# Kernel tuning notes

Hardware: AMD Instinct MI355X
Metric: run time of the kernel (lower is better)

The kernel has to match this reference:

```python
import jax, jax.numpy as jnp
import numpy as np

PZ = 16          # partition_size
SMOOTH = 1e-8


def setup_inputs() -> dict:
    key = jax.random.key(0)
    k1, k2, k3, k4 = jax.random.split(key, 4)
    shape = (4, 2, 160, 160, 160)  # [N, C, Z, X, Y]
    pred = jax.random.uniform(k1, shape, dtype=jnp.float32)
    groundtruth = jax.random.uniform(k2, shape, dtype=jnp.float32)
    a = jax.random.uniform(k3, (1,), dtype=jnp.float32)
    b = jax.random.uniform(k4, (1,), dtype=jnp.float32)
    return {"pred": pred, "groundtruth": groundtruth, "a": a, "b": b}


def _blocks(t):
    # [N,C,Z,X,Y] -> rows of per-(block, channel) voxels [N*nz*nx*ny*C, PZ^3]
    # matches the torch loops: blocks ordered (N, zz, xx, yy) with channel dim
    # of each block concatenated along dim 0 before flattening dims 1..-1.
    N, C, Z, X, Y = t.shape
    nz, nx, ny = Z // PZ, X // PZ, Y // PZ
    t = t.reshape(N, C, nz, PZ, nx, PZ, ny, PZ)
    t = t.transpose(0, 2, 4, 6, 1, 3, 5, 7)  # [N,nz,nx,ny,C,pz,pz,pz]
    return t.reshape(N * nz * nx * ny * C, PZ * PZ * PZ)


def reference(pred, groundtruth, a, b):
    p = _blocks(pred)
    g = _blocks(groundtruth)
    tp = jnp.sum(g * p, axis=1)
    fn = jnp.sum(g * (1.0 - p), axis=1)
    fp = jnp.sum((1.0 - g) * p, axis=1)
    denom = fp + fn + SMOOTH
    alpha = a + b * ((fp + SMOOTH) / denom)
    beta = a + b * ((fn + SMOOTH) / denom)
    loss = jnp.sum(1.0 - (tp + SMOOTH) / (tp + alpha * fp + beta * fn + SMOOTH))
    return loss
```

## Files before the change

kernel.cpp:

```cpp
#include <hip/hip_runtime.h>

#define SMOOTH 1e-8f

constexpr int NROWS = 8000;
constexpr int WG1   = 3200;

__global__ __launch_bounds__(256, 8)
void partial_kernel(const float* __restrict__ pred,
                    const float* __restrict__ gt,
                    float* __restrict__ wsq)
{
    int wg = blockIdx.x;
    const int q4 = wg & 3;  wg >>= 2;
    const int c  = wg & 1;  wg >>= 1;
    const int xx = wg % 10; wg /= 10;
    const int zz = wg % 10;
    const int n  = wg / 10;

    const int t  = threadIdx.x;
    const int s  = t & 15;
    const int xl = t >> 4;
    const long base0 =
        ((long)((n * 2 + c) * 160 + zz * 16 + q4 * 4) * 160 + xx * 16) * 40L;

    const float4* p4 = reinterpret_cast<const float4*>(pred);
    const float4* g4 = reinterpret_cast<const float4*>(gt);

    float S0 = 0, G0 = 0, P0 = 0;
    float S1 = 0, G1 = 0, P1 = 0;
    float S2 = 0, G2 = 0, P2 = 0;
    const bool j2 = (s < 8);

    #pragma unroll
    for (int plane = 0; plane < 4; ++plane) {
        const long lb = base0 + (long)plane * 6400 + xl * 40 + s;
        const float4 pa = p4[lb];      const float4 ga = g4[lb];
        const float4 pb = p4[lb + 16]; const float4 gb = g4[lb + 16];
        float4 pc, gc;
        if (j2) { pc = p4[lb + 32]; gc = g4[lb + 32]; }

        S0 += (pa.x + pa.y) + (pa.z + pa.w);
        G0 += (ga.x + ga.y) + (ga.z + ga.w);
        P0 += pa.x * ga.x + pa.y * ga.y + pa.z * ga.z + pa.w * ga.w;

        S1 += (pb.x + pb.y) + (pb.z + pb.w);
        G1 += (gb.x + gb.y) + (gb.z + gb.w);
        P1 += pb.x * gb.x + pb.y * gb.y + pb.z * gb.z + pb.w * gb.w;

        if (j2) {
            S2 += (pc.x + pc.y) + (pc.z + pc.w);
            G2 += (gc.x + gc.y) + (gc.z + gc.w);
            P2 += pc.x * gc.x + pc.y * gc.y + pc.z * gc.z + pc.w * gc.w;
        }
    }

#define RED4(x) x += __shfl_xor(x, 1, 64); x += __shfl_xor(x, 2, 64); \
                x += __shfl_xor(x, 16, 64); x += __shfl_xor(x, 32, 64);
    RED4(S0) RED4(G0) RED4(P0)
    RED4(S1) RED4(G1) RED4(P1)
    RED4(S2) RED4(G2) RED4(P2)
#undef RED4

    __shared__ float red[4][4][9];
    const int lane = t & 63, wave = t >> 6;
    if ((lane & 51) == 0) {
        const int q = lane >> 2;
        float* dst = red[wave][q];
        dst[0] = S0; dst[1] = G0; dst[2] = P0;
        dst[3] = S1; dst[4] = G1; dst[5] = P1;
        dst[6] = S2; dst[7] = G2; dst[8] = P2;
    }
    __syncthreads();

    if (t < 30) {
        const int yy   = t / 3;
        const int comp = t - yy * 3;
        const int q = yy & 3, j = yy >> 2;
        const float val = red[0][q][j * 3 + comp] + red[1][q][j * 3 + comp] +
                          red[2][q][j * 3 + comp] + red[3][q][j * 3 + comp];
        const int row = (((n * 10 + zz) * 10 + xx) * 10 + yy) * 2 + c;
        wsq[(row * 4 + q4) * 3 + comp] = val;
    }
}

__global__ __launch_bounds__(1024)
void finalize_kernel(const float* __restrict__ wsq,
                     const float* __restrict__ a_p,
                     const float* __restrict__ b_p,
                     float* __restrict__ out)
{
    const int t = threadIdx.x;
    const float a = a_p[0], b = b_p[0];
    float sum = 0.f;

    for (int r = t; r < NROWS; r += 1024) {
        const float4 w0 = *reinterpret_cast<const float4*>(wsq + r * 12);
        const float4 w1 = *reinterpret_cast<const float4*>(wsq + r * 12 + 4);
        const float4 w2 = *reinterpret_cast<const float4*>(wsq + r * 12 + 8);
        const float SP  = w0.x + w0.w + w1.z + w2.y;
        const float SG  = w0.y + w1.x + w1.w + w2.z;
        const float SGP = w0.z + w1.y + w2.x + w2.w;

        const float tp = SGP;
        const float fn = SG - SGP;
        const float fp = SP - SGP;
        const float denom = fp + fn + SMOOTH;
        const float alpha = a + b * ((fp + SMOOTH) / denom);
        const float beta  = a + b * ((fn + SMOOTH) / denom);
        sum += 1.f - (tp + SMOOTH) / (tp + alpha * fp + beta * fn + SMOOTH);
    }

    #pragma unroll
    for (int d = 32; d > 0; d >>= 1) sum += __shfl_down(sum, d, 64);

    __shared__ float wsum[16];
    if ((t & 63) == 0) wsum[t >> 6] = sum;
    __syncthreads();
    if (t == 0) {
        float tot = 0.f;
        #pragma unroll
        for (int i = 0; i < 16; ++i) tot += wsum[i];
        out[0] = tot;
    }
}

extern "C" void kernel_launch(void* const* d_in, const int* in_sizes, int n_in,
                              void* d_out, int out_size, void* d_ws, size_t ws_size,
                              hipStream_t stream)
{
    const float* pred = (const float*)d_in[0];
    const float* gt   = (const float*)d_in[1];
    const float* a_p  = (const float*)d_in[2];
    const float* b_p  = (const float*)d_in[3];
    float* out = (float*)d_out;
    float* wsq = (float*)d_ws;

    partial_kernel<<<WG1, 256, 0, stream>>>(pred, gt, wsq);
    finalize_kernel<<<1, 1024, 0, stream>>>(wsq, a_p, b_p, out);
}
```

Baseline: 302.6 us.

## Remap partial reduction so each wave streams one z-plane with nontemporal loads

Each wave now reads one contiguous z-plane slab (16 x-rows of 40 float4s) as 10 fully coalesced 64-lane float4 loads of pred and gt, all issued up front with nontemporal hints. Previously lanes were split by x-row and y-segment, with a predicated third load. The y-block assignment of each lane rotates across the 10 loads, so per-lane partials are regrouped into 5 y-block bins with selects before a cross-lane shuffle reduction and a smaller shared-memory combine. Occupancy hint drops to 4 waves-per-SIMD to allow the 80 live load registers, which trades latency hiding across waves for more memory-level parallelism per wave.

Result: faster. 252.8 us (-16.5%).

```diff
diff --git a/kernel.cpp b/kernel.cpp
--- a/kernel.cpp
+++ b/kernel.cpp
@@ -2,10 +2,12 @@
 
 #define SMOOTH 1e-8f
 
+typedef float f32x4 __attribute__((ext_vector_type(4)));
+
 constexpr int NROWS = 8000;
 constexpr int WG1   = 3200;
 
-__global__ __launch_bounds__(256, 8)
+__global__ __launch_bounds__(256, 4)
 void partial_kernel(const float* __restrict__ pred,
                     const float* __restrict__ gt,
                     float* __restrict__ wsq)
@@ -17,67 +19,83 @@
     const int zz = wg % 10;
     const int n  = wg / 10;
 
-    const int t  = threadIdx.x;
-    const int s  = t & 15;
-    const int xl = t >> 4;
-    const long base0 =
-        ((long)((n * 2 + c) * 160 + zz * 16 + q4 * 4) * 160 + xx * 16) * 40L;
+    const int t    = threadIdx.x;
+    const int lane = t & 63;
+    const int wave = t >> 6;
+    const int z    = zz * 16 + q4 * 4 + wave;
 
-    const float4* p4 = reinterpret_cast<const float4*>(pred);
-    const float4* g4 = reinterpret_cast<const float4*>(gt);
+    const long pb = ((long)((n * 2 + c) * 160 + z) * 160 + xx * 16) * 40L;
 
-    float S0 = 0, G0 = 0, P0 = 0;
-    float S1 = 0, G1 = 0, P1 = 0;
-    float S2 = 0, G2 = 0, P2 = 0;
-    const bool j2 = (s < 8);
+    const f32x4* p4 = reinterpret_cast<const f32x4*>(pred) + pb + lane;
+    const f32x4* g4 = reinterpret_cast<const f32x4*>(gt)  + pb + lane;
+
+    f32x4 P[10], G[10];
+    #pragma unroll
+    for (int k = 0; k < 10; ++k) {
+        P[k] = __builtin_nontemporal_load(p4 + k * 64);
+        G[k] = __builtin_nontemporal_load(g4 + k * 64);
+    }
+
+    float aS[5] = {0, 0, 0, 0, 0};
+    float aG[5] = {0, 0, 0, 0, 0};
+    float aP[5] = {0, 0, 0, 0, 0};
+    #pragma unroll
+    for (int k = 0; k < 10; ++k) {
+        const int m = k % 5;
+        const f32x4 p = P[k], g = G[k];
+        aS[m] += (p.x + p.y) + (p.z + p.w);
+        aG[m] += (g.x + g.y) + (g.z + g.w);
+        aP[m] += p.x * g.x + p.y * g.y + p.z * g.z + p.w * g.w;
+    }
+
+    int rr[5];
+    #pragma unroll
+    for (int m = 0; m < 5; ++m)
+        rr[m] = ((lane + 24 * m) % 40) >> 3;
+
+    float bS[5], bG[5], bP[5];
+    #pragma unroll
+    for (int r = 0; r < 5; ++r) {
+        float s = 0.f, g = 0.f, p = 0.f;
+        #pragma unroll
+        for (int m = 0; m < 5; ++m) {
+            const bool hit = (rr[m] == r);
+            s += hit ? aS[m] : 0.f;
+            g += hit ? aG[m] : 0.f;
+            p += hit ? aP[m] : 0.f;
+        }
+        bS[r] = s; bG[r] = g; bP[r] = p;
+    }
 
     #pragma unroll
-    for (int plane = 0; plane < 4; ++plane) {
-        const long lb = base0 + (long)plane * 6400 + xl * 40 + s;
-        const float4 pa = p4[lb];      const float4 ga = g4[lb];
-        const float4 pb = p4[lb + 16]; const float4 gb = g4[lb + 16];
-        float4 pc, gc;
-        if (j2) { pc = p4[lb + 32]; gc = g4[lb + 32]; }
-
-        S0 += (pa.x + pa.y) + (pa.z + pa.w);
-        G0 += (ga.x + ga.y) + (ga.z + ga.w);
-        P0 += pa.x * ga.x + pa.y * ga.y + pa.z * ga.z + pa.w * ga.w;
-
-        S1 += (pb.x + pb.y) + (pb.z + pb.w);
-        G1 += (gb.x + gb.y) + (gb.z + gb.w);
-        P1 += pb.x * gb.x + pb.y * gb.y + pb.z * gb.z + pb.w * gb.w;
-
-        if (j2) {
-            S2 += (pc.x + pc.y) + (pc.z + pc.w);
-            G2 += (gc.x + gc.y) + (gc.z + gc.w);
-            P2 += pc.x * gc.x + pc.y * gc.y + pc.z * gc.z + pc.w * gc.w;
+    for (int r = 0; r < 5; ++r) {
+        #pragma unroll
+        for (int d = 0; d < 5; ++d) {
+            const int msk = (d < 2) ? (1 << d) : (1 << (d + 1));
+            bS[r] += __shfl_xor(bS[r], msk, 64);
+            bG[r] += __shfl_xor(bG[r], msk, 64);
+            bP[r] += __shfl_xor(bP[r], msk, 64);
         }
     }
 
-#define RED4(x) x += __shfl_xor(x, 1, 64); x += __shfl_xor(x, 2, 64); \
-                x += __shfl_xor(x, 16, 64); x += __shfl_xor(x, 32, 64);
-    RED4(S0) RED4(G0) RED4(P0)
-    RED4(S1) RED4(G1) RED4(P1)
-    RED4(S2) RED4(G2) RED4(P2)
-#undef RED4
-
-    __shared__ float red[4][4][9];
-    const int lane = t & 63, wave = t >> 6;
-    if ((lane & 51) == 0) {
-        const int q = lane >> 2;
-        float* dst = red[wave][q];
-        dst[0] = S0; dst[1] = G0; dst[2] = P0;
-        dst[3] = S1; dst[4] = G1; dst[5] = P1;
-        dst[6] = S2; dst[7] = G2; dst[8] = P2;
+    __shared__ float red[4][2][15];
+    const int b = (lane >> 2) & 1;
+    if ((lane & 59) == 0) {
+        #pragma unroll
+        for (int r = 0; r < 5; ++r) {
+            red[wave][b][r * 3 + 0] = bS[r];
+            red[wave][b][r * 3 + 1] = bG[r];
+            red[wave][b][r * 3 + 2] = bP[r];
+        }
     }
     __syncthreads();
 
     if (t < 30) {
         const int yy   = t / 3;
         const int comp = t - yy * 3;
-        const int q = yy & 3, j = yy >> 2;
-        const float val = red[0][q][j * 3 + comp] + red[1][q][j * 3 + comp] +
-                          red[2][q][j * 3 + comp] + red[3][q][j * 3 + comp];
+        const int bb = yy & 1, r = yy >> 1;
+        const float val = red[0][bb][r * 3 + comp] + red[1][bb][r * 3 + comp] +
+                          red[2][bb][r * 3 + comp] + red[3][bb][r * 3 + comp];
         const int row = (((n * 10 + zz) * 10 + xx) * 10 + yy) * 2 + c;
         wsq[(row * 4 + q4) * 3 + comp] = val;
     }
```
